# Kernel optimization log

Measured on AMD Instinct MI355X. Metric: run time of the kernel, lower is better.

The kernel has to match this reference:

```python
import jax, jax.numpy as jnp
import numpy as np

N_NODES = 20000
N_EDGES = 320000
IN_F = 256
OUT_F = 256
EDGE_F = 256


def _mlp2(x, W1, b1, W2, b2):
    # MLPLayers(2, [d_in, 2*d_in, d_out]) = Linear -> ReLU -> Linear
    return jax.nn.relu(x @ W1 + b1) @ W2 + b2


def setup_inputs() -> dict:
    key = jax.random.key(0)
    ks = jax.random.split(key, 12)

    def lin(k, fan_in, shape):
        bound = 1.0 / np.sqrt(fan_in)
        return jax.random.uniform(k, shape, jnp.float32, -bound, bound)

    node_feat = jax.random.normal(ks[0], (N_NODES, IN_F), jnp.float32)
    edge_feat = jax.random.normal(ks[1], (N_EDGES, EDGE_F), jnp.float32)
    src = jax.random.randint(ks[2], (N_EDGES,), 0, N_NODES, jnp.int32)
    dst = jax.random.randint(ks[3], (N_EDGES,), 0, N_NODES, jnp.int32)

    # edge_mlp: edge_feats -> 2*edge_feats -> in_feats
    We1 = lin(ks[4], EDGE_F, (EDGE_F, 2 * EDGE_F))
    be1 = lin(ks[5], EDGE_F, (2 * EDGE_F,))
    We2 = lin(ks[6], 2 * EDGE_F, (2 * EDGE_F, IN_F))
    be2 = lin(ks[7], 2 * EDGE_F, (IN_F,))
    # node mlp: in_feats -> 2*in_feats -> out_feats
    Wn1 = lin(ks[8], IN_F, (IN_F, 2 * IN_F))
    bn1 = lin(ks[9], IN_F, (2 * IN_F,))
    Wn2 = lin(ks[10], 2 * IN_F, (2 * IN_F, OUT_F))
    bn2 = lin(ks[11], 2 * IN_F, (OUT_F,))
    eps = jnp.zeros((1,), jnp.float32)

    return {"node_feat": node_feat, "edge_feat": edge_feat, "src": src, "dst": dst,
            "We1": We1, "be1": be1, "We2": We2, "be2": be2,
            "Wn1": Wn1, "bn1": bn1, "Wn2": Wn2, "bn2": bn2, "eps": eps}


def reference(node_feat, edge_feat, src, dst, We1, be1, We2, be2, Wn1, bn1, Wn2, bn2, eps):
    e = _mlp2(edge_feat, We1, be1, We2, be2)            # [E, IN_F]
    msg = jax.nn.relu(node_feat[src] + e)               # gather-add-relu
    out_h = jax.ops.segment_sum(msg, dst, num_segments=N_NODES)  # [N, IN_F]
    out = _mlp2((1.0 + eps[0]) * node_feat + out_h, Wn1, bn1, Wn2, bn2)
    return out
```

## Files before the change

kernel.cpp:

```cpp
#include <hip/hip_runtime.h>
#include <hip/hip_bf16.h>

#define NN  20000
#define NE  320000
#define FIN 256
#define FH  512

typedef __attribute__((ext_vector_type(8))) short bf16x8;
typedef __attribute__((ext_vector_type(4))) float f32x4;
typedef __attribute__((ext_vector_type(4))) unsigned short u16x4;
typedef __attribute__((ext_vector_type(4))) unsigned int u32x4;

static __device__ __forceinline__ unsigned short f2b(float f) {
    union { float f; unsigned int i; } v; v.f = f;
    return (unsigned short)((v.i + 0x7fffu + ((v.i >> 16) & 1u)) >> 16);
}
static __device__ __forceinline__ f32x4 mfma16(bf16x8 a, bf16x8 b, f32x4 c) {
    return __builtin_amdgcn_mfma_f32_16x16x32_bf16(a, b, c, 0, 0, 0);
}
static __device__ __forceinline__ unsigned int cvtpk(float lo, float hi) {
    union { __hip_bfloat162 h; unsigned int u; } v;
    v.h = __float22bfloat162_rn(float2{lo, hi});
    return v.u;
}
static __device__ __forceinline__ u16x4 pack4(float a, float b, float c, float d) {
    union { u16x4 s; unsigned int u[2]; } v;
    v.u[0] = cvtpk(a, b); v.u[1] = cvtpk(c, d);
    return v.s;
}
static __device__ __forceinline__ bf16x8 cvt8(f32x4 a, f32x4 b) {
    u32x4 t;
    t[0] = cvtpk(a[0], a[1]);
    t[1] = cvtpk(a[2], a[3]);
    t[2] = cvtpk(b[0], b[1]);
    t[3] = cvtpk(b[2], b[3]);
    return __builtin_bit_cast(bf16x8, t);
}

__global__ void prep_weights(const float* __restrict__ We1, const float* __restrict__ We2,
                             const float* __restrict__ Wn1, const float* __restrict__ Wn2,
                             unsigned short* __restrict__ W1T, unsigned short* __restrict__ W2T,
                             unsigned short* __restrict__ Wn1T, unsigned short* __restrict__ Wn2T) {
    const int m = blockIdx.x >> 7;
    const int t = blockIdx.x & 127;
    const float* src; unsigned short* dst; int R, C;
    if      (m == 0) { src = We1; dst = W1T;  R = 256; C = 512; }
    else if (m == 1) { src = We2; dst = W2T;  R = 512; C = 256; }
    else if (m == 2) { src = Wn1; dst = Wn1T; R = 256; C = 512; }
    else             { src = Wn2; dst = Wn2T; R = 512; C = 256; }
    __shared__ unsigned short tl[32][33];
    const int tx  = threadIdx.x & 31;
    const int tyb = threadIdx.x >> 5;
    const int cb = C >> 5;
    const int bx = t % cb, by = t / cb;
    #pragma unroll
    for (int j = 0; j < 4; ++j)
        tl[tyb * 4 + j][tx] = f2b(src[(size_t)(by * 32 + tyb * 4 + j) * C + bx * 32 + tx]);
    __syncthreads();
    #pragma unroll
    for (int j = 0; j < 4; ++j)
        dst[(size_t)(bx * 32 + tyb * 4 + j) * R + by * 32 + tx] = tl[tx][tyb * 4 + j];
}

__global__ void hist_dst(const int* __restrict__ dstI, int* __restrict__ cnt) {
    int e = blockIdx.x * 256 + threadIdx.x;
    if (e < NE) atomicAdd(&cnt[dstI[e]], 1);
}

__global__ void scan_excl(const int* __restrict__ cnt, int* __restrict__ cursor) {
    __shared__ int c[NN];
    __shared__ int s[1024];
    const int t = threadIdx.x;
    for (int i = t; i < NN; i += 1024) c[i] = cnt[i];
    __syncthreads();
    const int lo = t * 20;
    const int hi = (lo + 20 < NN) ? lo + 20 : NN;
    int sum = 0;
    for (int i = lo; i < hi; ++i) sum += c[i];
    s[t] = sum;
    __syncthreads();
    for (int off = 1; off < 1024; off <<= 1) {
        int v = (t >= off) ? s[t - off] : 0;
        __syncthreads();
        s[t] += v;
        __syncthreads();
    }
    int base = (t > 0) ? s[t - 1] : 0;
    for (int i = lo; i < hi; ++i) { int cv = c[i]; c[i] = base; base += cv; }
    __syncthreads();
    for (int i = t; i < NN; i += 1024) cursor[i] = c[i];
}

__global__ void scatter_perm(const int* __restrict__ dstI,
                             int* __restrict__ cursor, int* __restrict__ perm) {
    int e = blockIdx.x * 256 + threadIdx.x;
    if (e < NE) {
        int pos = atomicAdd(&cursor[dstI[e]], 1);
        perm[pos] = e;
    }
}

__global__ void __launch_bounds__(512, 4)
gine_edge(const float* __restrict__ edge_feat,
          const float* __restrict__ node_feat,
          const int* __restrict__ srcI,
          const int* __restrict__ dstI,
          const int* __restrict__ perm,
          const unsigned short* __restrict__ W1T,
          const float* __restrict__ b1,
          const unsigned short* __restrict__ W2T,
          const float* __restrict__ b2,
          float* __restrict__ out_h)
{
    __shared__ union {
        unsigned short Xs[64 * 264];
        unsigned short Hs[64 * 512];
        float          Msg[64 * 260];
    } sh;
    __shared__ int snS[64], dnS[64], eS[64];

    const int tid  = threadIdx.x;
    const int wave = tid >> 6;
    const int lane = tid & 63;
    const int quad = lane >> 4;
    const int ln   = lane & 15;
    const int bs   = (blockIdx.x & 7) * 625 + (blockIdx.x >> 3);
    const int e0   = bs * 64;

    if (tid < 64) {
        const int e = perm[e0 + tid];
        eS[tid]  = e;
        snS[tid] = srcI[e];
        dnS[tid] = dstI[e];
    }
    __syncthreads();

    #pragma unroll
    for (int it = 0; it < 4; ++it) {
        const int chunk = tid + it * 512;
        const int row = chunk >> 5;
        const int c8  = (chunk & 31) << 3;
        const float* p = edge_feat + (size_t)eS[row] * FIN + c8;
        f32x4 o0 = *(const f32x4*)(p);
        f32x4 o1 = *(const f32x4*)(p + 4);
        *(bf16x8*)(&sh.Xs[row * 264 + c8]) = cvt8(o0, o1);
    }
    __syncthreads();

    f32x4 zero4 = {0.f, 0.f, 0.f, 0.f};
    f32x4 acc1[4][4];
    #pragma unroll
    for (int nt = 0; nt < 4; ++nt)
        #pragma unroll
        for (int et = 0; et < 4; ++et) acc1[nt][et] = zero4;

    const unsigned short* wB = W1T + (wave * 64 + ln) * FIN + quad * 8;
    __builtin_amdgcn_s_setprio(1);
    #pragma unroll
    for (int ks = 0; ks < 8; ++ks) {
        bf16x8 w[4], x[4];
        #pragma unroll
        for (int nt = 0; nt < 4; ++nt)
            w[nt] = *(const bf16x8*)(wB + nt * 16 * FIN + ks * 32);
        #pragma unroll
        for (int et = 0; et < 4; ++et)
            x[et] = *(const bf16x8*)(&sh.Xs[(et * 16 + ln) * 264 + quad * 8 + ks * 32]);
        #pragma unroll
        for (int nt = 0; nt < 4; ++nt)
            #pragma unroll
            for (int et = 0; et < 4; ++et)
                acc1[nt][et] = mfma16(w[nt], x[et], acc1[nt][et]);
    }
    __builtin_amdgcn_s_setprio(0);
    __syncthreads();

    #pragma unroll
    for (int nt = 0; nt < 4; ++nt) {
        const int n0 = wave * 64 + nt * 16 + quad * 4;
        const f32x4 b4 = *(const f32x4*)(b1 + n0);
        #pragma unroll
        for (int et = 0; et < 4; ++et) {
            const int edge = et * 16 + ln;
            u16x4 p = pack4(fmaxf(acc1[nt][et][0] + b4[0], 0.f),
                            fmaxf(acc1[nt][et][1] + b4[1], 0.f),
                            fmaxf(acc1[nt][et][2] + b4[2], 0.f),
                            fmaxf(acc1[nt][et][3] + b4[3], 0.f));
            *(u16x4*)(&sh.Hs[(edge << 9) + (((n0 >> 3) ^ (edge & 7)) << 3) + (n0 & 7)]) = p;
        }
    }
    __syncthreads();

    f32x4 acc2[2][4];
    #pragma unroll
    for (int nt = 0; nt < 2; ++nt)
        #pragma unroll
        for (int et = 0; et < 4; ++et) acc2[nt][et] = zero4;

    const unsigned short* w2B = W2T + (wave * 32 + ln) * FH;
    __builtin_amdgcn_s_setprio(1);
    #pragma unroll
    for (int ks = 0; ks < 16; ++ks) {
        const int kb = ks * 4 + quad;
        bf16x8 w[2], h[4];
        #pragma unroll
        for (int nt = 0; nt < 2; ++nt)
            w[nt] = *(const bf16x8*)(w2B + nt * 16 * FH + kb * 8);
        #pragma unroll
        for (int et = 0; et < 4; ++et) {
            const int edge = et * 16 + ln;
            h[et] = *(const bf16x8*)(&sh.Hs[(edge << 9) + ((kb ^ (edge & 7)) << 3)]);
        }
        #pragma unroll
        for (int nt = 0; nt < 2; ++nt)
            #pragma unroll
            for (int et = 0; et < 4; ++et)
                acc2[nt][et] = mfma16(w[nt], h[et], acc2[nt][et]);
    }
    __builtin_amdgcn_s_setprio(0);
    __syncthreads();

    #pragma unroll
    for (int nt = 0; nt < 2; ++nt) {
        const int n0 = wave * 32 + nt * 16 + quad * 4;
        const f32x4 b4 = *(const f32x4*)(b2 + n0);
        #pragma unroll
        for (int et = 0; et < 4; ++et) {
            const int edge = et * 16 + ln;
            const int sn = snS[edge];
            const f32x4 nf = *(const f32x4*)(node_feat + (size_t)sn * FIN + n0);
            f32x4 m;
            #pragma unroll
            for (int r = 0; r < 4; ++r)
                m[r] = fmaxf(nf[r] + acc2[nt][et][r] + b4[r], 0.f);
            *(f32x4*)(&sh.Msg[edge * 260 + n0]) = m;
        }
    }
    __syncthreads();

    {
        const int col  = tid & 255;
        const int half = tid >> 8;
        const int rA   = half * 32;
        const int dF = dnS[rA], dL = dnS[rA + 31];
        float run = sh.Msg[rA * 260 + col];
        int cur = dF;
        #pragma unroll 4
        for (int row = rA + 1; row < rA + 32; ++row) {
            const int d = dnS[row];
            if (d != cur) {
                if (cur == dF || cur == dL)
                    atomicAdd(&out_h[(size_t)cur * FIN + col], run);
                else
                    out_h[(size_t)cur * FIN + col] = run;
                run = 0.f;
                cur = d;
            }
            run += sh.Msg[row * 260 + col];
        }
        atomicAdd(&out_h[(size_t)cur * FIN + col], run);
    }
}

__global__ void __launch_bounds__(512, 4)
gine_node(const float* __restrict__ node_feat,
          const float* __restrict__ out_h,
          const unsigned short* __restrict__ W1T,
          const float* __restrict__ b1,
          const unsigned short* __restrict__ W2T,
          const float* __restrict__ b2,
          const float* __restrict__ eps,
          float* __restrict__ out)
{
    __shared__ union {
        unsigned short Xs[64 * 264];
        unsigned short Hs[64 * 512];
    } sh;

    const int tid  = threadIdx.x;
    const int wave = tid >> 6;
    const int lane = tid & 63;
    const int quad = lane >> 4;
    const int ln   = lane & 15;
    const int n0b  = blockIdx.x * 64;
    const float epsv = 1.0f + eps[0];

    #pragma unroll
    for (int it = 0; it < 4; ++it) {
        const int chunk = tid + it * 512;
        const int row = chunk >> 5;
        const int c8  = (chunk & 31) << 3;
        const int g   = n0b + row;
        bf16x8 pack = {0, 0, 0, 0, 0, 0, 0, 0};
        if (g < NN) {
            const float* pn = node_feat + (size_t)g * FIN + c8;
            const float* ph = out_h + (size_t)g * FIN + c8;
            f32x4 n0v = *(const f32x4*)(pn);
            f32x4 n1v = *(const f32x4*)(pn + 4);
            f32x4 h0v = *(const f32x4*)(ph);
            f32x4 h1v = *(const f32x4*)(ph + 4);
            f32x4 a, b;
            #pragma unroll
            for (int j = 0; j < 4; ++j) {
                a[j] = epsv * n0v[j] + h0v[j];
                b[j] = epsv * n1v[j] + h1v[j];
            }
            pack = cvt8(a, b);
        }
        *(bf16x8*)(&sh.Xs[row * 264 + c8]) = pack;
    }
    __syncthreads();

    f32x4 zero4 = {0.f, 0.f, 0.f, 0.f};
    f32x4 acc1[4][4];
    #pragma unroll
    for (int nt = 0; nt < 4; ++nt)
        #pragma unroll
        for (int et = 0; et < 4; ++et) acc1[nt][et] = zero4;

    const unsigned short* wB = W1T + (wave * 64 + ln) * FIN + quad * 8;
    __builtin_amdgcn_s_setprio(1);
    #pragma unroll
    for (int ks = 0; ks < 8; ++ks) {
        bf16x8 w[4], xv[4];
        #pragma unroll
        for (int nt = 0; nt < 4; ++nt)
            w[nt] = *(const bf16x8*)(wB + nt * 16 * FIN + ks * 32);
        #pragma unroll
        for (int et = 0; et < 4; ++et)
            xv[et] = *(const bf16x8*)(&sh.Xs[(et * 16 + ln) * 264 + quad * 8 + ks * 32]);
        #pragma unroll
        for (int nt = 0; nt < 4; ++nt)
            #pragma unroll
            for (int et = 0; et < 4; ++et)
                acc1[nt][et] = mfma16(w[nt], xv[et], acc1[nt][et]);
    }
    __builtin_amdgcn_s_setprio(0);
    __syncthreads();

    #pragma unroll
    for (int nt = 0; nt < 4; ++nt) {
        const int n0 = wave * 64 + nt * 16 + quad * 4;
        const f32x4 b4 = *(const f32x4*)(b1 + n0);
        #pragma unroll
        for (int et = 0; et < 4; ++et) {
            const int edge = et * 16 + ln;
            u16x4 p = pack4(fmaxf(acc1[nt][et][0] + b4[0], 0.f),
                            fmaxf(acc1[nt][et][1] + b4[1], 0.f),
                            fmaxf(acc1[nt][et][2] + b4[2], 0.f),
                            fmaxf(acc1[nt][et][3] + b4[3], 0.f));
            *(u16x4*)(&sh.Hs[(edge << 9) + (((n0 >> 3) ^ (edge & 7)) << 3) + (n0 & 7)]) = p;
        }
    }
    __syncthreads();

    f32x4 acc2[2][4];
    #pragma unroll
    for (int nt = 0; nt < 2; ++nt)
        #pragma unroll
        for (int et = 0; et < 4; ++et) acc2[nt][et] = zero4;

    const unsigned short* w2B = W2T + (wave * 32 + ln) * FH;
    __builtin_amdgcn_s_setprio(1);
    #pragma unroll
    for (int ks = 0; ks < 16; ++ks) {
        const int kb = ks * 4 + quad;
        bf16x8 w[2], h[4];
        #pragma unroll
        for (int nt = 0; nt < 2; ++nt)
            w[nt] = *(const bf16x8*)(w2B + nt * 16 * FH + kb * 8);
        #pragma unroll
        for (int et = 0; et < 4; ++et) {
            const int edge = et * 16 + ln;
            h[et] = *(const bf16x8*)(&sh.Hs[(edge << 9) + ((kb ^ (edge & 7)) << 3)]);
        }
        #pragma unroll
        for (int nt = 0; nt < 2; ++nt)
            #pragma unroll
            for (int et = 0; et < 4; ++et)
                acc2[nt][et] = mfma16(w[nt], h[et], acc2[nt][et]);
    }
    __builtin_amdgcn_s_setprio(0);

    #pragma unroll
    for (int nt = 0; nt < 2; ++nt) {
        const int n0 = wave * 32 + nt * 16 + quad * 4;
        const f32x4 b4 = *(const f32x4*)(b2 + n0);
        #pragma unroll
        for (int et = 0; et < 4; ++et) {
            const int g = n0b + et * 16 + ln;
            if (g < NN) {
                f32x4 o;
                #pragma unroll
                for (int r = 0; r < 4; ++r)
                    o[r] = acc2[nt][et][r] + b4[r];
                *(f32x4*)(out + (size_t)g * FIN + n0) = o;
            }
        }
    }
}

extern "C" void kernel_launch(void* const* d_in, const int* in_sizes, int n_in,
                              void* d_out, int out_size, void* d_ws, size_t ws_size,
                              hipStream_t stream) {
    const float* node_feat = (const float*)d_in[0];
    const float* edge_feat = (const float*)d_in[1];
    const int* srcI = (const int*)d_in[2];
    const int* dstI = (const int*)d_in[3];
    const float* We1 = (const float*)d_in[4];
    const float* be1 = (const float*)d_in[5];
    const float* We2 = (const float*)d_in[6];
    const float* be2 = (const float*)d_in[7];
    const float* Wn1 = (const float*)d_in[8];
    const float* bn1 = (const float*)d_in[9];
    const float* Wn2 = (const float*)d_in[10];
    const float* bn2 = (const float*)d_in[11];
    const float* eps = (const float*)d_in[12];

    char* ws = (char*)d_ws;
    float* out_h = (float*)ws;
    unsigned short* W1T  = (unsigned short*)(ws + 20480000);
    unsigned short* W2T  = W1T + 131072;
    unsigned short* Wn1T = W2T + 131072;
    unsigned short* Wn2T = Wn1T + 131072;
    int* cnt    = (int*)(ws + 20480000 + 4 * 262144);
    int* cursor = cnt + NN;
    int* perm   = cursor + NN;

    hipMemsetAsync(out_h, 0, (size_t)NN * FIN * sizeof(float), stream);
    hipMemsetAsync(cnt, 0, NN * sizeof(int), stream);

    prep_weights<<<512, 256, 0, stream>>>(We1, We2, Wn1, Wn2, W1T, W2T, Wn1T, Wn2T);

    hist_dst<<<(NE + 255) / 256, 256, 0, stream>>>(dstI, cnt);
    scan_excl<<<1, 1024, 0, stream>>>(cnt, cursor);
    scatter_perm<<<(NE + 255) / 256, 256, 0, stream>>>(dstI, cursor, perm);

    gine_edge<<<NE / 64, 512, 0, stream>>>(edge_feat, node_feat, srcI, dstI,
                                           perm, W1T, be1, W2T, be2, out_h);
    gine_node<<<(NN + 63) / 64, 512, 0, stream>>>(node_feat, out_h, Wn1T, bn1,
                                                  Wn2T, bn2, eps, (float*)d_out);
}
```

Measured before the change: 865.3 us.

## Pre-pack weights into MFMA fragment order and prefetch gathered node features

Weights are now repacked into per-lane MFMA fragment order so each wave's weight load is one contiguous 16-byte-per-lane read instead of strided row accesses. The edge kernel drops the initial perm/src/dst staging barrier by reading perm directly in the feature-gather loop. It also issues the node_feat gathers before the second GEMM so their latency overlaps with MFMA work. The cost is extra live registers for the prefetched node features, which may affect occupancy.

```diff
diff --git a/kernel.cpp b/kernel.cpp
--- a/kernel.cpp
+++ b/kernel.cpp
@@ -39,27 +39,29 @@
 
 __global__ void prep_weights(const float* __restrict__ We1, const float* __restrict__ We2,
                              const float* __restrict__ Wn1, const float* __restrict__ Wn2,
-                             unsigned short* __restrict__ W1T, unsigned short* __restrict__ W2T,
-                             unsigned short* __restrict__ Wn1T, unsigned short* __restrict__ Wn2T) {
-    const int m = blockIdx.x >> 7;
-    const int t = blockIdx.x & 127;
-    const float* src; unsigned short* dst; int R, C;
-    if      (m == 0) { src = We1; dst = W1T;  R = 256; C = 512; }
-    else if (m == 1) { src = We2; dst = W2T;  R = 512; C = 256; }
-    else if (m == 2) { src = Wn1; dst = Wn1T; R = 256; C = 512; }
-    else             { src = Wn2; dst = Wn2T; R = 512; C = 256; }
-    __shared__ unsigned short tl[32][33];
-    const int tx  = threadIdx.x & 31;
-    const int tyb = threadIdx.x >> 5;
-    const int cb = C >> 5;
-    const int bx = t % cb, by = t / cb;
-    #pragma unroll
-    for (int j = 0; j < 4; ++j)
-        tl[tyb * 4 + j][tx] = f2b(src[(size_t)(by * 32 + tyb * 4 + j) * C + bx * 32 + tx]);
-    __syncthreads();
-    #pragma unroll
-    for (int j = 0; j < 4; ++j)
-        dst[(size_t)(bx * 32 + tyb * 4 + j) * R + by * 32 + tx] = tl[tx][tyb * 4 + j];
+                             unsigned short* __restrict__ W1F, unsigned short* __restrict__ W2F,
+                             unsigned short* __restrict__ Wn1F, unsigned short* __restrict__ Wn2F) {
+    const int b = blockIdx.x;
+    const int m = b >> 8;
+    const int f = b & 255;
+    const float* src; unsigned short* dst; int N, K;
+    if      (m == 0) { src = We1; dst = W1F;  N = 512; K = 256; }
+    else if (m == 1) { src = We2; dst = W2F;  N = 256; K = 512; }
+    else if (m == 2) { src = Wn1; dst = Wn1F; N = 512; K = 256; }
+    else             { src = Wn2; dst = Wn2F; N = 256; K = 512; }
+    const int KB  = K >> 5;
+    const int nf  = f / KB, ks = f % KB;
+    const int l   = threadIdx.x;
+    const int quad = l >> 4, ln = l & 15;
+    const int n  = nf * 16 + ln;
+    const int k0 = ks * 32 + quad * 8;
+    f32x4 a, c;
+    #pragma unroll
+    for (int j = 0; j < 4; ++j) {
+        a[j] = src[(size_t)(k0 + j) * N + n];
+        c[j] = src[(size_t)(k0 + 4 + j) * N + n];
+    }
+    *(bf16x8*)(dst + ((size_t)f * 64 + l) * 8) = cvt8(a, c);
 }
 
 __global__ void hist_dst(const int* __restrict__ dstI, int* __restrict__ cnt) {
@@ -106,9 +108,9 @@
           const int* __restrict__ srcI,
           const int* __restrict__ dstI,
           const int* __restrict__ perm,
-          const unsigned short* __restrict__ W1T,
+          const unsigned short* __restrict__ W1F,
           const float* __restrict__ b1,
-          const unsigned short* __restrict__ W2T,
+          const unsigned short* __restrict__ W2F,
           const float* __restrict__ b2,
           float* __restrict__ out_h)
 {
@@ -117,7 +119,7 @@
         unsigned short Hs[64 * 512];
         float          Msg[64 * 260];
     } sh;
-    __shared__ int snS[64], dnS[64], eS[64];
+    __shared__ int snS[64], dnS[64];
 
     const int tid  = threadIdx.x;
     const int wave = tid >> 6;
@@ -127,24 +129,22 @@
     const int bs   = (blockIdx.x & 7) * 625 + (blockIdx.x >> 3);
     const int e0   = bs * 64;
 
-    if (tid < 64) {
-        const int e = perm[e0 + tid];
-        eS[tid]  = e;
-        snS[tid] = srcI[e];
-        dnS[tid] = dstI[e];
-    }
-    __syncthreads();
-
     #pragma unroll
     for (int it = 0; it < 4; ++it) {
         const int chunk = tid + it * 512;
         const int row = chunk >> 5;
         const int c8  = (chunk & 31) << 3;
-        const float* p = edge_feat + (size_t)eS[row] * FIN + c8;
+        const int e   = perm[e0 + row];
+        const float* p = edge_feat + (size_t)e * FIN + c8;
         f32x4 o0 = *(const f32x4*)(p);
         f32x4 o1 = *(const f32x4*)(p + 4);
         *(bf16x8*)(&sh.Xs[row * 264 + c8]) = cvt8(o0, o1);
     }
+    if (tid < 64) {
+        const int e = perm[e0 + tid];
+        snS[tid] = srcI[e];
+        dnS[tid] = dstI[e];
+    }
     __syncthreads();
 
     f32x4 zero4 = {0.f, 0.f, 0.f, 0.f};
@@ -154,14 +154,13 @@
         #pragma unroll
         for (int et = 0; et < 4; ++et) acc1[nt][et] = zero4;
 
-    const unsigned short* wB = W1T + (wave * 64 + ln) * FIN + quad * 8;
     __builtin_amdgcn_s_setprio(1);
     #pragma unroll
     for (int ks = 0; ks < 8; ++ks) {
         bf16x8 w[4], x[4];
         #pragma unroll
         for (int nt = 0; nt < 4; ++nt)
-            w[nt] = *(const bf16x8*)(wB + nt * 16 * FIN + ks * 32);
+            w[nt] = *(const bf16x8*)(W1F + (((wave * 4 + nt) * 8 + ks) * 64 + lane) * 8);
         #pragma unroll
         for (int et = 0; et < 4; ++et)
             x[et] = *(const bf16x8*)(&sh.Xs[(et * 16 + ln) * 264 + quad * 8 + ks * 32]);
@@ -190,13 +189,23 @@
     }
     __syncthreads();
 
+    f32x4 nfr[2][4];
+    #pragma unroll
+    for (int nt = 0; nt < 2; ++nt) {
+        const int n0 = wave * 32 + nt * 16 + quad * 4;
+        #pragma unroll
+        for (int et = 0; et < 4; ++et) {
+            const int sn = snS[et * 16 + ln];
+            nfr[nt][et] = *(const f32x4*)(node_feat + (size_t)sn * FIN + n0);
+        }
+    }
+
     f32x4 acc2[2][4];
     #pragma unroll
     for (int nt = 0; nt < 2; ++nt)
         #pragma unroll
         for (int et = 0; et < 4; ++et) acc2[nt][et] = zero4;
 
-    const unsigned short* w2B = W2T + (wave * 32 + ln) * FH;
     __builtin_amdgcn_s_setprio(1);
     #pragma unroll
     for (int ks = 0; ks < 16; ++ks) {
@@ -204,7 +213,7 @@
         bf16x8 w[2], h[4];
         #pragma unroll
         for (int nt = 0; nt < 2; ++nt)
-            w[nt] = *(const bf16x8*)(w2B + nt * 16 * FH + kb * 8);
+            w[nt] = *(const bf16x8*)(W2F + (((wave * 2 + nt) * 16 + ks) * 64 + lane) * 8);
         #pragma unroll
         for (int et = 0; et < 4; ++et) {
             const int edge = et * 16 + ln;
@@ -226,12 +235,10 @@
         #pragma unroll
         for (int et = 0; et < 4; ++et) {
             const int edge = et * 16 + ln;
-            const int sn = snS[edge];
-            const f32x4 nf = *(const f32x4*)(node_feat + (size_t)sn * FIN + n0);
             f32x4 m;
             #pragma unroll
             for (int r = 0; r < 4; ++r)
-                m[r] = fmaxf(nf[r] + acc2[nt][et][r] + b4[r], 0.f);
+                m[r] = fmaxf(nfr[nt][et][r] + acc2[nt][et][r] + b4[r], 0.f);
             *(f32x4*)(&sh.Msg[edge * 260 + n0]) = m;
         }
     }
@@ -264,9 +271,9 @@
 __global__ void __launch_bounds__(512, 4)
 gine_node(const float* __restrict__ node_feat,
           const float* __restrict__ out_h,
-          const unsigned short* __restrict__ W1T,
+          const unsigned short* __restrict__ W1F,
           const float* __restrict__ b1,
-          const unsigned short* __restrict__ W2T,
+          const unsigned short* __restrict__ W2F,
           const float* __restrict__ b2,
           const float* __restrict__ eps,
           float* __restrict__ out)
@@ -317,14 +324,13 @@
         #pragma unroll
         for (int et = 0; et < 4; ++et) acc1[nt][et] = zero4;
 
-    const unsigned short* wB = W1T + (wave * 64 + ln) * FIN + quad * 8;
     __builtin_amdgcn_s_setprio(1);
     #pragma unroll
     for (int ks = 0; ks < 8; ++ks) {
         bf16x8 w[4], xv[4];
         #pragma unroll
         for (int nt = 0; nt < 4; ++nt)
-            w[nt] = *(const bf16x8*)(wB + nt * 16 * FIN + ks * 32);
+            w[nt] = *(const bf16x8*)(W1F + (((wave * 4 + nt) * 8 + ks) * 64 + lane) * 8);
         #pragma unroll
         for (int et = 0; et < 4; ++et)
             xv[et] = *(const bf16x8*)(&sh.Xs[(et * 16 + ln) * 264 + quad * 8 + ks * 32]);
@@ -359,7 +365,6 @@
         #pragma unroll
         for (int et = 0; et < 4; ++et) acc2[nt][et] = zero4;
 
-    const unsigned short* w2B = W2T + (wave * 32 + ln) * FH;
     __builtin_amdgcn_s_setprio(1);
     #pragma unroll
     for (int ks = 0; ks < 16; ++ks) {
@@ -367,7 +372,7 @@
         bf16x8 w[2], h[4];
         #pragma unroll
         for (int nt = 0; nt < 2; ++nt)
-            w[nt] = *(const bf16x8*)(w2B + nt * 16 * FH + kb * 8);
+            w[nt] = *(const bf16x8*)(W2F + (((wave * 2 + nt) * 16 + ks) * 64 + lane) * 8);
         #pragma unroll
         for (int et = 0; et < 4; ++et) {
             const int edge = et * 16 + ln;
@@ -418,10 +423,10 @@
 
     char* ws = (char*)d_ws;
     float* out_h = (float*)ws;
-    unsigned short* W1T  = (unsigned short*)(ws + 20480000);
-    unsigned short* W2T  = W1T + 131072;
-    unsigned short* Wn1T = W2T + 131072;
-    unsigned short* Wn2T = Wn1T + 131072;
+    unsigned short* W1F  = (unsigned short*)(ws + 20480000);
+    unsigned short* W2F  = W1F + 131072;
+    unsigned short* Wn1F = W2F + 131072;
+    unsigned short* Wn2F = Wn1F + 131072;
     int* cnt    = (int*)(ws + 20480000 + 4 * 262144);
     int* cursor = cnt + NN;
     int* perm   = cursor + NN;
@@ -429,14 +434,14 @@
     hipMemsetAsync(out_h, 0, (size_t)NN * FIN * sizeof(float), stream);
     hipMemsetAsync(cnt, 0, NN * sizeof(int), stream);
 
-    prep_weights<<<512, 256, 0, stream>>>(We1, We2, Wn1, Wn2, W1T, W2T, Wn1T, Wn2T);
+    prep_weights<<<1024, 64, 0, stream>>>(We1, We2, Wn1, Wn2, W1F, W2F, Wn1F, Wn2F);
 
     hist_dst<<<(NE + 255) / 256, 256, 0, stream>>>(dstI, cnt);
     scan_excl<<<1, 1024, 0, stream>>>(cnt, cursor);
     scatter_perm<<<(NE + 255) / 256, 256, 0, stream>>>(dstI, cursor, perm);
 
     gine_edge<<<NE / 64, 512, 0, stream>>>(edge_feat, node_feat, srcI, dstI,
-                                           perm, W1T, be1, W2T, be2, out_h);
-    gine_node<<<(NN + 63) / 64, 512, 0, stream>>>(node_feat, out_h, Wn1T, bn1,
-                                                  Wn2T, bn2, eps, (float*)d_out);
-}
+                                           perm, W1F, be1, W2F, be2, out_h);
+    gine_node<<<(NN + 63) / 64, 512, 0, stream>>>(node_feat, out_h, Wn1F, bn1,
+                                                  Wn2F, bn2, eps, (float*)d_out);
+}
```

Measured after the change: 820.8 us. 1.05x faster.
